# Kernel tuning notes

Measured on AMD Instinct MI355X. Metric: run time of the kernel, lower is better.

## Reference

```python
import jax, jax.numpy as jnp
import numpy as np

H = 16
EPS = 1e-5

def _layernorm(x, gamma, beta):
    mu = jnp.mean(x, axis=-1, keepdims=True)
    var = jnp.var(x, axis=-1, keepdims=True)
    return (x - mu) * jax.lax.rsqrt(var + EPS) * gamma + beta

def setup_inputs() -> dict:
    key = jax.random.key(0)
    ks = jax.random.split(key, 5)
    B, T, E = 4, 2048, 1024
    D = E // H
    return {
        "x": jax.random.normal(ks[0], (B, T, E), dtype=jnp.float32),
        "Wqkv": jax.random.normal(ks[1], (E, 3 * E), dtype=jnp.float32) * (E ** -0.5),
        "bqkv": jax.random.normal(ks[2], (3 * E,), dtype=jnp.float32) * 0.02,
        "q_gamma": jnp.ones((D,), jnp.float32),
        "q_beta": jnp.zeros((D,), jnp.float32),
        "k_gamma": jnp.ones((D,), jnp.float32),
        "k_beta": jnp.zeros((D,), jnp.float32),
        "Wproj": jax.random.normal(ks[3], (E, E), dtype=jnp.float32) * (E ** -0.5),
        "bproj": jnp.zeros((E,), jnp.float32),
    }

def reference(x, Wqkv, bqkv, q_gamma, q_beta, k_gamma, k_beta, Wproj, bproj):
    B, T, E = x.shape
    D = E // H
    qkv = x @ Wqkv + bqkv                      # [B,T,3E]
    q, k, v = jnp.split(qkv, 3, axis=-1)
    # b t (h d) -> b h t d
    to_heads = lambda a: a.reshape(B, T, H, D).transpose(0, 2, 1, 3)
    q, k, v = to_heads(q), to_heads(k), to_heads(v)
    q = _layernorm(q, q_gamma, q_beta)
    k = _layernorm(k, k_gamma, k_beta)
    scale = 1.0 / jnp.sqrt(jnp.float32(D))
    scores = jnp.einsum('bhtd,bhsd->bhts', q, k) * scale   # [B,H,T,T]
    attn = jax.nn.softmax(scores, axis=-1)
    y = jnp.einsum('bhts,bhsd->bhtd', attn, v)             # [B,H,T,D]
    y = y.transpose(0, 2, 1, 3).reshape(B, T, E)           # b h t d -> b t (h d)
    return y @ Wproj + bproj
```

## Files before the change

### kernel.cpp

```cpp
#include <hip/hip_runtime.h>

#define Hn  16
#define Dh  64
#define Bb  4
#define Tn  2048
#define En  1024
#define Mn  8192
#define N1  3072
#define Kn  1024

typedef __attribute__((ext_vector_type(8)))  short  short8;
typedef __attribute__((ext_vector_type(4)))  short  short4v;
typedef __attribute__((ext_vector_type(4)))  float  f32x4;
typedef __attribute__((ext_vector_type(8)))  __bf16 bf16x8;

__device__ __forceinline__ float b2f(short s) {
  unsigned u = ((unsigned)(unsigned short)s) << 16;
  return __builtin_bit_cast(float, u);
}
__device__ __forceinline__ short f2b(float f) {
  unsigned u = __builtin_bit_cast(unsigned, f);
  u += 0x7fffu + ((u >> 16) & 1u);
  return (short)(u >> 16);
}
__device__ __forceinline__ f32x4 mfma16(short8 a, short8 b, f32x4 c) {
  return __builtin_amdgcn_mfma_f32_16x16x32_bf16(
      __builtin_bit_cast(bf16x8, a), __builtin_bit_cast(bf16x8, b), c, 0, 0, 0);
}
__device__ __forceinline__ void gload16(const void* g, void* l) {
  __builtin_amdgcn_global_load_lds(
      (const __attribute__((address_space(1))) unsigned int*)g,
      (__attribute__((address_space(3))) unsigned int*)l, 16, 0, 0);
}

__global__ __launch_bounds__(256) void prep_kernel(
    const float* __restrict__ x, short* __restrict__ xb,
    const float* __restrict__ Wqkv, short* __restrict__ wqkvT,
    const float* __restrict__ Wproj, short* __restrict__ wprojT) {
  __shared__ float tile[32][33];
  const int bid = blockIdx.x, tid = threadIdx.x;
  if (bid < 4096) {
    const size_t i = ((size_t)bid * 256 + tid) * 8;
    f32x4 a = *(const f32x4*)&x[i];
    f32x4 b = *(const f32x4*)&x[i + 4];
    short8 o;
    o[0]=f2b(a[0]); o[1]=f2b(a[1]); o[2]=f2b(a[2]); o[3]=f2b(a[3]);
    o[4]=f2b(b[0]); o[5]=f2b(b[1]); o[6]=f2b(b[2]); o[7]=f2b(b[3]);
    *(short8*)&xb[i] = o;
    return;
  }
  const float* in; short* out; int R, C, bx, by;
  if (bid < 4096 + 3072) {
    const int b2 = bid - 4096;
    in = Wqkv; out = wqkvT; R = Kn; C = N1; bx = b2 % 96; by = b2 / 96;
  } else {
    const int b3 = bid - 7168;
    in = Wproj; out = wprojT; R = Kn; C = En; bx = b3 % 32; by = b3 / 32;
  }
  const int c0 = bx * 32, r0 = by * 32;
  const int lr = tid >> 3, lc = (tid & 7) * 4;
  f32x4 v = *(const f32x4*)&in[(size_t)(r0 + lr) * C + c0 + lc];
  tile[lr][lc] = v[0]; tile[lr][lc+1] = v[1]; tile[lr][lc+2] = v[2]; tile[lr][lc+3] = v[3];
  __syncthreads();
  const int oc = tid >> 3, orr = (tid & 7) * 4;
  short4v ov;
  ov[0] = f2b(tile[orr][oc]);   ov[1] = f2b(tile[orr+1][oc]);
  ov[2] = f2b(tile[orr+2][oc]); ov[3] = f2b(tile[orr+3][oc]);
  *(short4v*)&out[(size_t)(c0 + oc) * R + r0 + orr] = ov;
}

template<int MODE>
__global__ __launch_bounds__(256) void gemm_kernel(
    const short* __restrict__ A, const short* __restrict__ Bt,
    const float* __restrict__ bias, float* __restrict__ Cf,
    short* __restrict__ qo, short* __restrict__ ko2, short* __restrict__ vo,
    const float* __restrict__ qg, const float* __restrict__ qb,
    const float* __restrict__ kg, const float* __restrict__ kb,
    int N, int NBX, int cpx) {
  __shared__ short S[8192];
  const int lin = blockIdx.x;
  const int swz = (lin & 7) * cpx + (lin >> 3);
  const int bx = swz % NBX, by = swz / NBX;
  const int tid = threadIdx.x, lane = tid & 63, w = tid >> 6;
  const int rowBase = by * 128, colBase = bx * 128;
  f32x4 acc[4][4] = {};
  const int srow = tid >> 2, sk = (tid & 3) << 3;
  const short* Ag = A  + (size_t)(rowBase + srow) * Kn + sk;
  const short* Bg = Bt + (size_t)(colBase + srow) * Kn + sk;
  short* AsW = S + w * 512;
  short* BsW = S + 4096 + w * 512;
  const int ar = (w >> 1) * 64, bc = (w & 1) * 64;
  const int lg = lane >> 4, lg8 = lg * 8, lr = lane & 15;

  for (int kt = 0; kt < Kn; kt += 32) {
    __syncthreads();
    gload16(Ag + kt,            AsW);
    gload16(Ag + kt + 64 * Kn,  AsW + 2048);
    gload16(Bg + kt,            BsW);
    gload16(Bg + kt + 64 * Kn,  BsW + 2048);
    __syncthreads();
    short8 af[4], bfr[4];
#pragma unroll
    for (int m = 0; m < 4; ++m) af[m]  = *(const short8*)&S[(ar + m*16 + lr)*32 + lg8];
#pragma unroll
    for (int n = 0; n < 4; ++n) bfr[n] = *(const short8*)&S[4096 + (bc + n*16 + lr)*32 + lg8];
#pragma unroll
    for (int m = 0; m < 4; ++m)
#pragma unroll
      for (int n = 0; n < 4; ++n)
        acc[m][n] = mfma16(af[m], bfr[n], acc[m][n]);
  }

  const int gr0 = rowBase + ar + lg * 4;
  const int gc0 = colBase + bc + lr;

  float bb[4];
#pragma unroll
  for (int n = 0; n < 4; ++n) bb[n] = bias[gc0 + n * 16];
#pragma unroll
  for (int m = 0; m < 4; ++m)
#pragma unroll
    for (int n = 0; n < 4; ++n)
#pragma unroll
      for (int r = 0; r < 4; ++r) acc[m][n][r] += bb[n];

  if (MODE == 0) {
#pragma unroll
    for (int m = 0; m < 4; ++m)
#pragma unroll
      for (int n = 0; n < 4; ++n) {
        const int gc = gc0 + n * 16;
#pragma unroll
        for (int r = 0; r < 4; ++r)
          Cf[(size_t)(gr0 + m*16 + r) * N + gc] = acc[m][n][r];
      }
    return;
  }

  const int which = colBase >> 10;
  if (which < 2) {
    const float* gp = (which == 0) ? qg : kg;
    const float* bp = (which == 0) ? qb : kb;
    const float sc = (which == 0) ? 0.1803368801111204f : 1.0f;
    float gam[4], bet[4];
#pragma unroll
    for (int n = 0; n < 4; ++n) { gam[n] = gp[n * 16 + lr]; bet[n] = bp[n * 16 + lr]; }
#pragma unroll
    for (int m = 0; m < 4; ++m)
#pragma unroll
      for (int r = 0; r < 4; ++r) {
        float s1 = 0.f, s2 = 0.f;
#pragma unroll
        for (int n = 0; n < 4; ++n) {
          const float v = acc[m][n][r];
          s1 += v; s2 += v * v;
        }
#pragma unroll
        for (int off = 1; off < 16; off <<= 1) {
          s1 += __shfl_xor(s1, off);
          s2 += __shfl_xor(s2, off);
        }
        const float mu = s1 * 0.015625f;
        const float rs = rsqrtf(s2 * 0.015625f - mu * mu + 1e-5f);
#pragma unroll
        for (int n = 0; n < 4; ++n)
          acc[m][n][r] = ((acc[m][n][r] - mu) * rs * gam[n] + bet[n]) * sc;
      }
  }

  __syncthreads();
  short* Sw = S + w * 2048;
  const int t0 = (rowBase & 2047) + ar;
  const int bidx = (rowBase + ar) >> 11;
  const int hh = ((colBase + bc) & 1023) >> 6;
  const int bh = bidx * Hn + hh;
  const int l8 = lane & 7, ld8 = lane >> 3;

  if (which < 2) {
    short* dst0 = (which == 0) ? qo : ko2;
#pragma unroll
    for (int p = 0; p < 2; ++p) {
#pragma unroll
      for (int mm = 0; mm < 2; ++mm) {
        const int m = p * 2 + mm;
#pragma unroll
        for (int n = 0; n < 4; ++n)
#pragma unroll
          for (int r = 0; r < 4; ++r) {
            const int tl = mm*16 + lg*4 + r;
            const int dl = n*16 + lr;
            Sw[tl*64 + (dl ^ ((tl & 7) << 3))] = f2b(acc[m][n][r]);
          }
      }
#pragma unroll
      for (int i = 0; i < 4; ++i) {
        const int tl = i*8 + ld8;
        short8 v = *(const short8*)&Sw[tl*64 + ((l8*8) ^ ((tl & 7) << 3))];
        const int t = t0 + p*32 + tl;
        *(short8*)&dst0[((size_t)bh * Tn + t) * Dh + l8*8] = v;
      }
    }
  } else {
#pragma unroll
    for (int p = 0; p < 2; ++p) {
#pragma unroll
      for (int nn = 0; nn < 2; ++nn) {
        const int n = p * 2 + nn;
#pragma unroll
        for (int m = 0; m < 4; ++m)
#pragma unroll
          for (int r = 0; r < 4; ++r) {
            const int dl = nn*16 + lr;
            const int tc = m*16 + lg*4 + r;
            Sw[dl*64 + (tc ^ ((dl & 7) << 3))] = f2b(acc[m][n][r]);
          }
      }
#pragma unroll
      for (int i = 0; i < 4; ++i) {
        const int dl = i*8 + ld8;
        short8 v = *(const short8*)&Sw[dl*64 + ((l8*8) ^ ((dl & 7) << 3))];
        const int d = p*32 + dl;
        *(short8*)&vo[((size_t)bh * Dh + d) * Tn + t0 + l8*8] = v;
      }
    }
  }
}

__global__ __launch_bounds__(256) void flash_kernel(
    const short* __restrict__ qp, const short* __restrict__ kp,
    const short* __restrict__ vt, short* __restrict__ y) {
  __shared__ short Ks[2][4096];
  __shared__ short Vs[2][4096];
  __shared__ short Ps[4096];
  const int tid = threadIdx.x, lane = tid & 63, w = tid >> 6;
  const int lr = lane & 15, lg = lane >> 4;

  const int j0 = blockIdx.x;
  const int xcd = j0 & 7, kk0 = j0 >> 3;
  const int bh = 8 * xcd + (kk0 & 7), qt = kk0 >> 3;

  const int qrow0 = qt * 128 + w * 32;
  const short* qbase = qp + ((size_t)bh * Tn + qrow0) * Dh;

  short8 aq[2][2];
#pragma unroll
  for (int m = 0; m < 2; ++m)
#pragma unroll
    for (int kk = 0; kk < 2; ++kk)
      aq[m][kk] = *(const short8*)&qbase[(m*16 + lr)*64 + kk*32 + lg*8];

  short8 ones;
#pragma unroll
  for (int i = 0; i < 8; ++i) ones[i] = (short)0x3F80;

  f32x4 o[2][4] = {};
  f32x4 lacc[2] = {};
  float mrow[2][4];
#pragma unroll
  for (int m = 0; m < 2; ++m)
#pragma unroll
    for (int r = 0; r < 4; ++r) mrow[m][r] = -3e38f;

  const int srow = tid >> 3;
  const int sc = (tid & 7) * 8;
  short* Pw = Ps + w * 1024;
  const short* kb = kp + (size_t)bh * Tn * Dh;
  const short* vb = vt + (size_t)bh * Dh * Tn;

#define STAGE(jt, bsel)                                                   \
  {                                                                       \
    _Pragma("unroll")                                                     \
    for (int i = 0; i < 2; ++i) {                                         \
      const int row = i * 32 + srow;                                      \
      const int scs = sc ^ ((row & 7) << 3);                              \
      gload16(kb + (size_t)((jt) * 64 + row) * Dh + scs,                  \
              &Ks[bsel][w * 512 + i * 2048]);                             \
      gload16(vb + (size_t)row * Tn + (jt) * 64 + scs,                    \
              &Vs[bsel][w * 512 + i * 2048]);                             \
    }                                                                     \
  }

#define PSW(q) ((((q) & 3) << 3) ^ (((q) & 4) << 2))

  STAGE(0, 0);
  __syncthreads();

  for (int j = 0; j < Tn / 64; ++j) {
    const int cur = j & 1;
    if (j + 1 < Tn / 64) STAGE(j + 1, cur ^ 1);

    short8 bk[4][2];
#pragma unroll
    for (int n = 0; n < 4; ++n)
#pragma unroll
      for (int kk = 0; kk < 2; ++kk) {
        const int row = n * 16 + lr;
        bk[n][kk] = *(const short8*)&Ks[cur][row*64 + ((kk*32 + lg*8) ^ ((row & 7) << 3))];
      }
    f32x4 s[2][4] = {};
    __builtin_amdgcn_s_setprio(1);
#pragma unroll
    for (int m = 0; m < 2; ++m)
#pragma unroll
      for (int n = 0; n < 4; ++n) {
        s[m][n] = mfma16(aq[m][0], bk[n][0], s[m][n]);
        s[m][n] = mfma16(aq[m][1], bk[n][1], s[m][n]);
      }
    __builtin_amdgcn_s_setprio(0);

    float pm[2][4];
#pragma unroll
    for (int m = 0; m < 2; ++m)
#pragma unroll
      for (int r = 0; r < 4; ++r)
        pm[m][r] = fmaxf(fmaxf(s[m][0][r], s[m][1][r]), fmaxf(s[m][2][r], s[m][3][r]));
    int ok = 1;
#pragma unroll
    for (int m = 0; m < 2; ++m)
#pragma unroll
      for (int r = 0; r < 4; ++r)
        ok &= (pm[m][r] <= mrow[m][r] + 11.0f) ? 1 : 0;
    if (!__all(ok)) {
      float tm[2][4];
#pragma unroll
      for (int m = 0; m < 2; ++m)
#pragma unroll
        for (int r = 0; r < 4; ++r) tm[m][r] = pm[m][r];
#pragma unroll
      for (int off = 1; off < 16; off <<= 1)
#pragma unroll
        for (int m = 0; m < 2; ++m)
#pragma unroll
          for (int r = 0; r < 4; ++r)
            tm[m][r] = fmaxf(tm[m][r], __shfl_xor(tm[m][r], off));
#pragma unroll
      for (int m = 0; m < 2; ++m)
#pragma unroll
        for (int r = 0; r < 4; ++r) {
          const float mn = fmaxf(mrow[m][r], tm[m][r]);
          const float corr = __builtin_amdgcn_exp2f(mrow[m][r] - mn);
          lacc[m][r] *= corr;
#pragma unroll
          for (int dn = 0; dn < 4; ++dn) o[m][dn][r] *= corr;
          mrow[m][r] = mn;
        }
    }

    short8 bv[4][2];
#pragma unroll
    for (int dn = 0; dn < 4; ++dn)
#pragma unroll
      for (int kk = 0; kk < 2; ++kk) {
        const int row = dn * 16 + lr;
        bv[dn][kk] = *(const short8*)&Vs[cur][row*64 + ((kk*32 + lg*8) ^ ((row & 7) << 3))];
      }

    __syncthreads();

#pragma unroll
    for (int m = 0; m < 2; ++m)
#pragma unroll
      for (int n = 0; n < 2; ++n)
#pragma unroll
        for (int r = 0; r < 4; ++r) {
          const float p = __builtin_amdgcn_exp2f(s[m][n][r] - mrow[m][r]);
          const unsigned u = __builtin_bit_cast(unsigned, p);
          const int q = m*16 + lg*4 + r;
          Pw[q*32 + ((n*16 + lr) ^ PSW(q))] = (short)(u >> 16);
        }
    short8 pa0[2];
#pragma unroll
    for (int m = 0; m < 2; ++m) {
      const int q = m*16 + lr;
      pa0[m] = *(const short8*)&Pw[q*32 + ((lg*8) ^ PSW(q))];
    }
    __builtin_amdgcn_s_setprio(1);
#pragma unroll
    for (int m = 0; m < 2; ++m) {
      lacc[m] = mfma16(pa0[m], ones, lacc[m]);
#pragma unroll
      for (int dn = 0; dn < 4; ++dn)
        o[m][dn] = mfma16(pa0[m], bv[dn][0], o[m][dn]);
    }
    __builtin_amdgcn_s_setprio(0);

#pragma unroll
    for (int m = 0; m < 2; ++m)
#pragma unroll
      for (int n = 0; n < 2; ++n)
#pragma unroll
        for (int r = 0; r < 4; ++r) {
          const float p = __builtin_amdgcn_exp2f(s[m][2 + n][r] - mrow[m][r]);
          const unsigned u = __builtin_bit_cast(unsigned, p);
          const int q = m*16 + lg*4 + r;
          Pw[q*32 + ((n*16 + lr) ^ PSW(q))] = (short)(u >> 16);
        }
    short8 pa1[2];
#pragma unroll
    for (int m = 0; m < 2; ++m) {
      const int q = m*16 + lr;
      pa1[m] = *(const short8*)&Pw[q*32 + ((lg*8) ^ PSW(q))];
    }
    __builtin_amdgcn_s_setprio(1);
#pragma unroll
    for (int m = 0; m < 2; ++m) {
      lacc[m] = mfma16(pa1[m], ones, lacc[m]);
#pragma unroll
      for (int dn = 0; dn < 4; ++dn)
        o[m][dn] = mfma16(pa1[m], bv[dn][1], o[m][dn]);
    }
    __builtin_amdgcn_s_setprio(0);
  }
#undef STAGE
#undef PSW

  const int b = bh >> 4, hh = bh & 15;
  short* yb = y + (size_t)b * Tn * En + hh * 64;
#pragma unroll
  for (int m = 0; m < 2; ++m)
#pragma unroll
    for (int r = 0; r < 4; ++r) {
      const float rl = 1.0f / lacc[m][r];
      const int t = qrow0 + m*16 + lg*4 + r;
#pragma unroll
      for (int dn = 0; dn < 4; ++dn) {
        const int d = dn*16 + lr;
        yb[(size_t)t * En + d] = f2b(o[m][dn][r] * rl);
      }
    }
}

extern "C" void kernel_launch(void* const* d_in, const int* in_sizes, int n_in,
                              void* d_out, int out_size, void* d_ws, size_t ws_size,
                              hipStream_t stream) {
  const float* x     = (const float*)d_in[0];
  const float* Wqkv  = (const float*)d_in[1];
  const float* bqkv  = (const float*)d_in[2];
  const float* qg    = (const float*)d_in[3];
  const float* qb    = (const float*)d_in[4];
  const float* kg    = (const float*)d_in[5];
  const float* kb    = (const float*)d_in[6];
  const float* Wproj = (const float*)d_in[7];
  const float* bproj = (const float*)d_in[8];
  float* out = (float*)d_out;

  char* p = (char*)d_ws;
  short* xb     = (short*)p; p += (size_t)Mn * Kn * 2;
  short* wqkvT  = (short*)p; p += (size_t)N1 * Kn * 2;
  short* wprojT = (short*)p; p += (size_t)En * Kn * 2;
  short* qp     = (short*)p; p += (size_t)Mn * Kn * 2;
  short* kp     = (short*)p; p += (size_t)Mn * Kn * 2;
  short* vtb    = (short*)p; p += (size_t)Mn * Kn * 2;
  short* yb     = (short*)p; p += (size_t)Mn * Kn * 2;

  prep_kernel<<<8192, 256, 0, stream>>>(x, xb, Wqkv, wqkvT, Wproj, wprojT);
  gemm_kernel<1><<<(N1 / 128) * (Mn / 128), 256, 0, stream>>>(
      xb, wqkvT, bqkv, nullptr, qp, kp, vtb, qg, qb, kg, kb,
      N1, N1 / 128, (N1 / 128) * (Mn / 128) / 8);
  flash_kernel<<<1024, 256, 0, stream>>>(qp, kp, vtb, yb);
  gemm_kernel<0><<<(En / 128) * (Mn / 128), 256, 0, stream>>>(
      yb, wprojT, bproj, out, nullptr, nullptr, nullptr, nullptr, nullptr, nullptr, nullptr,
      En, En / 128, (En / 128) * (Mn / 128) / 8);
}
```

Baseline: 245.6 us.

## Rewrite flash attention with 32x32x16 MFMA and transposed S=K·Q layout

Replaces the 16x16x32 MFMA flash kernel with one built on 32x32x16 bf16 MFMA. It computes S transposed (K as the A operand, Q held in registers as B), so each lane owns one query row. The row max and row sum then become in-register reductions plus a single cross-half shuffle, instead of 16-lane butterfly shuffles and a ones-vector MFMA for the denominator. P is repacked to bf16 through lane shuffles rather than a round trip through an LDS scratch buffer, which removes the Ps buffer. The trade-offs are a larger per-lane accumulator footprint and shuffle-heavy repacking, with possible register pressure.

```diff
diff --git a/kernel.cpp b/kernel.cpp
--- a/kernel.cpp
+++ b/kernel.cpp
@@ -12,7 +12,10 @@
 typedef __attribute__((ext_vector_type(8)))  short  short8;
 typedef __attribute__((ext_vector_type(4)))  short  short4v;
 typedef __attribute__((ext_vector_type(4)))  float  f32x4;
+typedef __attribute__((ext_vector_type(16))) float  f32x16;
 typedef __attribute__((ext_vector_type(8)))  __bf16 bf16x8;
+typedef __attribute__((ext_vector_type(4)))  int    i32x4;
+typedef __attribute__((ext_vector_type(2)))  int    i32x2;
 
 __device__ __forceinline__ float b2f(short s) {
   unsigned u = ((unsigned)(unsigned short)s) << 16;
@@ -27,10 +30,27 @@
   return __builtin_amdgcn_mfma_f32_16x16x32_bf16(
       __builtin_bit_cast(bf16x8, a), __builtin_bit_cast(bf16x8, b), c, 0, 0, 0);
 }
+__device__ __forceinline__ f32x16 mfma32(short8 a, short8 b, f32x16 c) {
+  return __builtin_amdgcn_mfma_f32_32x32x16_bf16(
+      __builtin_bit_cast(bf16x8, a), __builtin_bit_cast(bf16x8, b), c, 0, 0, 0);
+}
 __device__ __forceinline__ void gload16(const void* g, void* l) {
   __builtin_amdgcn_global_load_lds(
       (const __attribute__((address_space(1))) unsigned int*)g,
       (__attribute__((address_space(3))) unsigned int*)l, 16, 0, 0);
+}
+__device__ __forceinline__ float vmax16(f32x16 v) {
+  float a0 = fmaxf(v[0], v[1]),   a1 = fmaxf(v[2], v[3]);
+  float a2 = fmaxf(v[4], v[5]),   a3 = fmaxf(v[6], v[7]);
+  float a4 = fmaxf(v[8], v[9]),   a5 = fmaxf(v[10], v[11]);
+  float a6 = fmaxf(v[12], v[13]), a7 = fmaxf(v[14], v[15]);
+  float b0 = fmaxf(a0, a1), b1 = fmaxf(a2, a3), b2 = fmaxf(a4, a5), b3 = fmaxf(a6, a7);
+  return fmaxf(fmaxf(b0, b1), fmaxf(b2, b3));
+}
+__device__ __forceinline__ float vsum16(f32x16 v) {
+  float a0 = v[0]+v[1], a1 = v[2]+v[3], a2 = v[4]+v[5], a3 = v[6]+v[7];
+  float a4 = v[8]+v[9], a5 = v[10]+v[11], a6 = v[12]+v[13], a7 = v[14]+v[15];
+  return ((a0+a1)+(a2+a3)) + ((a4+a5)+(a6+a7));
 }
 
 __global__ __launch_bounds__(256) void prep_kernel(
@@ -226,61 +246,47 @@
   }
 }
 
-__global__ __launch_bounds__(256) void flash_kernel(
+__global__ __launch_bounds__(256) void flash32_kernel(
     const short* __restrict__ qp, const short* __restrict__ kp,
     const short* __restrict__ vt, short* __restrict__ y) {
-  __shared__ short Ks[2][4096];
-  __shared__ short Vs[2][4096];
-  __shared__ short Ps[4096];
-  const int tid = threadIdx.x, lane = tid & 63, w = tid >> 6;
-  const int lr = lane & 15, lg = lane >> 4;
+  __shared__ char lds[32768];
+  char* ldsK = lds;
+  char* ldsV = lds + 16384;
+
+  const int tid = threadIdx.x, l = tid & 63, w = tid >> 6;
+  const int l31 = l & 31, hi = l >> 5;
 
   const int j0 = blockIdx.x;
   const int xcd = j0 & 7, kk0 = j0 >> 3;
   const int bh = 8 * xcd + (kk0 & 7), qt = kk0 >> 3;
 
   const int qrow0 = qt * 128 + w * 32;
-  const short* qbase = qp + ((size_t)bh * Tn + qrow0) * Dh;
-
-  short8 aq[2][2];
-#pragma unroll
-  for (int m = 0; m < 2; ++m)
-#pragma unroll
-    for (int kk = 0; kk < 2; ++kk)
-      aq[m][kk] = *(const short8*)&qbase[(m*16 + lr)*64 + kk*32 + lg*8];
-
-  short8 ones;
-#pragma unroll
-  for (int i = 0; i < 8; ++i) ones[i] = (short)0x3F80;
-
-  f32x4 o[2][4] = {};
-  f32x4 lacc[2] = {};
-  float mrow[2][4];
-#pragma unroll
-  for (int m = 0; m < 2; ++m)
-#pragma unroll
-    for (int r = 0; r < 4; ++r) mrow[m][r] = -3e38f;
-
-  const int srow = tid >> 3;
-  const int sc = (tid & 7) * 8;
-  short* Pw = Ps + w * 1024;
-  const short* kb = kp + (size_t)bh * Tn * Dh;
-  const short* vb = vt + (size_t)bh * Dh * Tn;
-
-#define STAGE(jt, bsel)                                                   \
-  {                                                                       \
-    _Pragma("unroll")                                                     \
-    for (int i = 0; i < 2; ++i) {                                         \
-      const int row = i * 32 + srow;                                      \
-      const int scs = sc ^ ((row & 7) << 3);                              \
-      gload16(kb + (size_t)((jt) * 64 + row) * Dh + scs,                  \
-              &Ks[bsel][w * 512 + i * 2048]);                             \
-      gload16(vb + (size_t)row * Tn + (jt) * 64 + scs,                    \
-              &Vs[bsel][w * 512 + i * 2048]);                             \
-    }                                                                     \
-  }
-
-#define PSW(q) ((((q) & 3) << 3) ^ (((q) & 4) << 2))
+  const short* qrow = qp + ((size_t)bh * Tn + qrow0 + l31) * Dh;
+  short8 qf[4];
+#pragma unroll
+  for (int c = 0; c < 4; ++c)
+    qf[c] = *(const short8*)&qrow[c * 16 + hi * 8];
+
+  f32x16 o[2] = {};
+  float m = -1e30f, lsum = 0.f;
+
+  const char* kb2 = (const char*)(kp + (size_t)bh * Tn * Dh);
+  const char* vb2 = (const char*)(vt + (size_t)bh * Dh * Tn);
+  const int sr0 = tid >> 3;
+  const int colb = (tid & 7) << 4;
+
+#define STAGE(jt, bsel)                                                          \
+  {                                                                              \
+    _Pragma("unroll")                                                            \
+    for (int i = 0; i < 2; ++i) {                                                \
+      const int row = i * 32 + sr0;                                              \
+      const int sw = colb ^ ((row & 7) << 4);                                    \
+      gload16(kb2 + (size_t)((jt) * 64 + row) * 128 + sw,                        \
+              ldsK + (bsel) * 8192 + i * 4096 + tid * 16);                       \
+      gload16(vb2 + (size_t)row * (Tn * 2) + (size_t)(jt) * 128 + sw,            \
+              ldsV + (bsel) * 8192 + i * 4096 + tid * 16);                       \
+    }                                                                            \
+  }
 
   STAGE(0, 0);
   __syncthreads();
@@ -289,144 +295,95 @@
     const int cur = j & 1;
     if (j + 1 < Tn / 64) STAGE(j + 1, cur ^ 1);
 
-    short8 bk[4][2];
-#pragma unroll
-    for (int n = 0; n < 4; ++n)
-#pragma unroll
-      for (int kk = 0; kk < 2; ++kk) {
-        const int row = n * 16 + lr;
-        bk[n][kk] = *(const short8*)&Ks[cur][row*64 + ((kk*32 + lg*8) ^ ((row & 7) << 3))];
-      }
-    f32x4 s[2][4] = {};
+    const char* Kb = ldsK + cur * 8192;
+    const char* Vb = ldsV + cur * 8192;
+
+    f32x16 p[2] = {};
     __builtin_amdgcn_s_setprio(1);
 #pragma unroll
-    for (int m = 0; m < 2; ++m)
-#pragma unroll
-      for (int n = 0; n < 4; ++n) {
-        s[m][n] = mfma16(aq[m][0], bk[n][0], s[m][n]);
-        s[m][n] = mfma16(aq[m][1], bk[n][1], s[m][n]);
-      }
+    for (int t = 0; t < 2; ++t) {
+      const int row = t * 32 + l31;
+#pragma unroll
+      for (int c = 0; c < 4; ++c) {
+        short8 a = *(const short8*)(Kb + row * 128 + ((c * 32 + hi * 16) ^ ((row & 7) << 4)));
+        p[t] = mfma32(a, qf[c], p[t]);
+      }
+    }
     __builtin_amdgcn_s_setprio(0);
 
-    float pm[2][4];
-#pragma unroll
-    for (int m = 0; m < 2; ++m)
-#pragma unroll
-      for (int r = 0; r < 4; ++r)
-        pm[m][r] = fmaxf(fmaxf(s[m][0][r], s[m][1][r]), fmaxf(s[m][2][r], s[m][3][r]));
-    int ok = 1;
-#pragma unroll
-    for (int m = 0; m < 2; ++m)
-#pragma unroll
-      for (int r = 0; r < 4; ++r)
-        ok &= (pm[m][r] <= mrow[m][r] + 11.0f) ? 1 : 0;
-    if (!__all(ok)) {
-      float tm[2][4];
-#pragma unroll
-      for (int m = 0; m < 2; ++m)
-#pragma unroll
-        for (int r = 0; r < 4; ++r) tm[m][r] = pm[m][r];
-#pragma unroll
-      for (int off = 1; off < 16; off <<= 1)
-#pragma unroll
-        for (int m = 0; m < 2; ++m)
-#pragma unroll
-          for (int r = 0; r < 4; ++r)
-            tm[m][r] = fmaxf(tm[m][r], __shfl_xor(tm[m][r], off));
-#pragma unroll
-      for (int m = 0; m < 2; ++m)
-#pragma unroll
-        for (int r = 0; r < 4; ++r) {
-          const float mn = fmaxf(mrow[m][r], tm[m][r]);
-          const float corr = __builtin_amdgcn_exp2f(mrow[m][r] - mn);
-          lacc[m][r] *= corr;
-#pragma unroll
-          for (int dn = 0; dn < 4; ++dn) o[m][dn][r] *= corr;
-          mrow[m][r] = mn;
+    float mx = fmaxf(vmax16(p[0]), vmax16(p[1]));
+    mx = fmaxf(mx, __shfl_xor(mx, 32));
+    if (!__all(mx - m <= 11.0f)) {
+      const float mn = fmaxf(m, mx);
+      const float corr = __builtin_amdgcn_exp2f(m - mn);
+      lsum *= corr;
+      o[0] *= corr;
+      o[1] *= corr;
+      m = mn;
+    }
+#pragma unroll
+    for (int t = 0; t < 2; ++t)
+#pragma unroll
+      for (int e = 0; e < 16; ++e)
+        p[t][e] = __builtin_amdgcn_exp2f(p[t][e] - m);
+    {
+      float ps = vsum16(p[0]) + vsum16(p[1]);
+      lsum += ps + __shfl_xor(ps, 32);
+    }
+
+    short8 pf[4];
+#pragma unroll
+    for (int t = 0; t < 2; ++t) {
+      float ex[16];
+#pragma unroll
+      for (int r = 0; r < 16; ++r) ex[r] = __shfl_xor(p[t][r], 32);
+#pragma unroll
+      for (int f = 0; f < 2; ++f) {
+        const int rb = 8 * f;
+        float sl[8];
+#pragma unroll
+        for (int jj = 0; jj < 4; ++jj) sl[jj]     = (hi == 0) ? p[t][rb + jj]     : ex[rb + 4 + jj];
+#pragma unroll
+        for (int jj = 4; jj < 8; ++jj) sl[jj]     = (hi == 0) ? ex[rb + jj - 4]   : p[t][rb + jj];
+        i32x4 wv;
+#pragma unroll
+        for (int i = 0; i < 4; ++i) {
+          const unsigned lo = __builtin_bit_cast(unsigned, sl[2*i])     >> 16;
+          const unsigned hw = __builtin_bit_cast(unsigned, sl[2*i + 1]) & 0xffff0000u;
+          wv[i] = (int)(hw | lo);
         }
-    }
-
-    short8 bv[4][2];
-#pragma unroll
-    for (int dn = 0; dn < 4; ++dn)
-#pragma unroll
-      for (int kk = 0; kk < 2; ++kk) {
-        const int row = dn * 16 + lr;
-        bv[dn][kk] = *(const short8*)&Vs[cur][row*64 + ((kk*32 + lg*8) ^ ((row & 7) << 3))];
-      }
+        pf[2*t + f] = __builtin_bit_cast(short8, wv);
+      }
+    }
+
+    __builtin_amdgcn_s_setprio(1);
+#pragma unroll
+    for (int dt = 0; dt < 2; ++dt) {
+      const int row = dt * 32 + l31;
+#pragma unroll
+      for (int c = 0; c < 4; ++c) {
+        short8 a = *(const short8*)(Vb + row * 128 + ((c * 32 + hi * 16) ^ ((row & 7) << 4)));
+        o[dt] = mfma32(a, pf[c], o[dt]);
+      }
+    }
+    __builtin_amdgcn_s_setprio(0);
 
     __syncthreads();
-
-#pragma unroll
-    for (int m = 0; m < 2; ++m)
-#pragma unroll
-      for (int n = 0; n < 2; ++n)
-#pragma unroll
-        for (int r = 0; r < 4; ++r) {
-          const float p = __builtin_amdgcn_exp2f(s[m][n][r] - mrow[m][r]);
-          const unsigned u = __builtin_bit_cast(unsigned, p);
-          const int q = m*16 + lg*4 + r;
-          Pw[q*32 + ((n*16 + lr) ^ PSW(q))] = (short)(u >> 16);
-        }
-    short8 pa0[2];
-#pragma unroll
-    for (int m = 0; m < 2; ++m) {
-      const int q = m*16 + lr;
-      pa0[m] = *(const short8*)&Pw[q*32 + ((lg*8) ^ PSW(q))];
-    }
-    __builtin_amdgcn_s_setprio(1);
-#pragma unroll
-    for (int m = 0; m < 2; ++m) {
-      lacc[m] = mfma16(pa0[m], ones, lacc[m]);
-#pragma unroll
-      for (int dn = 0; dn < 4; ++dn)
-        o[m][dn] = mfma16(pa0[m], bv[dn][0], o[m][dn]);
-    }
-    __builtin_amdgcn_s_setprio(0);
-
-#pragma unroll
-    for (int m = 0; m < 2; ++m)
-#pragma unroll
-      for (int n = 0; n < 2; ++n)
-#pragma unroll
-        for (int r = 0; r < 4; ++r) {
-          const float p = __builtin_amdgcn_exp2f(s[m][2 + n][r] - mrow[m][r]);
-          const unsigned u = __builtin_bit_cast(unsigned, p);
-          const int q = m*16 + lg*4 + r;
-          Pw[q*32 + ((n*16 + lr) ^ PSW(q))] = (short)(u >> 16);
-        }
-    short8 pa1[2];
-#pragma unroll
-    for (int m = 0; m < 2; ++m) {
-      const int q = m*16 + lr;
-      pa1[m] = *(const short8*)&Pw[q*32 + ((lg*8) ^ PSW(q))];
-    }
-    __builtin_amdgcn_s_setprio(1);
-#pragma unroll
-    for (int m = 0; m < 2; ++m) {
-      lacc[m] = mfma16(pa1[m], ones, lacc[m]);
-#pragma unroll
-      for (int dn = 0; dn < 4; ++dn)
-        o[m][dn] = mfma16(pa1[m], bv[dn][1], o[m][dn]);
-    }
-    __builtin_amdgcn_s_setprio(0);
   }
 #undef STAGE
-#undef PSW
-
+
+  const float rl = 1.0f / lsum;
   const int b = bh >> 4, hh = bh & 15;
-  short* yb = y + (size_t)b * Tn * En + hh * 64;
-#pragma unroll
-  for (int m = 0; m < 2; ++m)
-#pragma unroll
-    for (int r = 0; r < 4; ++r) {
-      const float rl = 1.0f / lacc[m][r];
-      const int t = qrow0 + m*16 + lg*4 + r;
-#pragma unroll
-      for (int dn = 0; dn < 4; ++dn) {
-        const int d = dn*16 + lr;
-        yb[(size_t)t * En + d] = f2b(o[m][dn][r] * rl);
-      }
+  const int t = qrow0 + l31;
+  short* yrow = y + ((size_t)(b * Tn + t)) * En + hh * 64;
+#pragma unroll
+  for (int dt = 0; dt < 2; ++dt)
+#pragma unroll
+    for (int g = 0; g < 4; ++g) {
+      short4v v4;
+#pragma unroll
+      for (int i = 0; i < 4; ++i) v4[i] = f2b(o[dt][g*4 + i] * rl);
+      *(short4v*)&yrow[dt*32 + g*8 + hi*4] = v4;
     }
 }
 
@@ -457,7 +414,7 @@
   gemm_kernel<1><<<(N1 / 128) * (Mn / 128), 256, 0, stream>>>(
       xb, wqkvT, bqkv, nullptr, qp, kp, vtb, qg, qb, kg, kb,
       N1, N1 / 128, (N1 / 128) * (Mn / 128) / 8);
-  flash_kernel<<<1024, 256, 0, stream>>>(qp, kp, vtb, yb);
+  flash32_kernel<<<1024, 256, 0, stream>>>(qp, kp, vtb, yb);
   gemm_kernel<0><<<(En / 128) * (Mn / 128), 256, 0, stream>>>(
       yb, wprojT, bproj, out, nullptr, nullptr, nullptr, nullptr, nullptr, nullptr, nullptr,
       En, En / 128, (En / 128) * (Mn / 128) / 8);
```

After: 257.2 us. +4.7%, slower.
